# Performance work log

Hardware: AMD Instinct MI355X
Metric: run time of the kernel (lower is better)

Reference implementation:

```python
import jax, jax.numpy as jnp
import numpy as np

B, C, L = 64, 50, 128      # tactic states, context entries per state, AST tokens per entry
V, S = 100008, 128          # vocab (sum of id tables), state/embed dim
OUT = 3


def _gru(h, x, w_ih, w_hh, b_ih, b_hh):
    # torch.nn.GRUCell math
    gi = x @ w_ih.T + b_ih            # [N, 3S]
    gh = h @ w_hh.T + b_hh
    i_r, i_z, i_n = jnp.split(gi, 3, axis=-1)
    h_r, h_z, h_n = jnp.split(gh, 3, axis=-1)
    r = jax.nn.sigmoid(i_r + h_r)
    z = jax.nn.sigmoid(i_z + h_z)
    n = jnp.tanh(i_n + r * h_n)
    return (1.0 - z) * n + z * h


def setup_inputs() -> dict:
    key = jax.random.key(0)
    ks = jax.random.split(key, 16)
    def nrm(k, shape, scale=0.05):
        return jax.random.normal(k, shape, dtype=jnp.float32) * scale
    return {
        "token_ids": jax.random.randint(ks[0], (B, C, L), 0, V),
        "embed_table": nrm(ks[1], (V, S)),
        "ast_w_ih": nrm(ks[2], (3 * S, S)),
        "ast_w_hh": nrm(ks[3], (3 * S, S)),
        "ast_b_ih": nrm(ks[4], (3 * S,)),
        "ast_b_hh": nrm(ks[5], (3 * S,)),
        "ast_init": nrm(ks[6], (1, S)),
        "ctx_w_ih": nrm(ks[7], (3 * S, S)),
        "ctx_w_hh": nrm(ks[8], (3 * S, S)),
        "ctx_b_ih": nrm(ks[9], (3 * S,)),
        "ctx_b_hh": nrm(ks[10], (3 * S,)),
        "ctx_init": nrm(ks[11], (1, S)),
        "proj_w": nrm(ks[12], (S, S + 1)),
        "proj_b": nrm(ks[13], (S,)),
        "final_w": nrm(ks[14], (OUT, S)),
        "final_b": nrm(ks[15], (OUT,)),
    }


def reference(token_ids, embed_table, ast_w_ih, ast_w_hh, ast_b_ih, ast_b_hh,
              ast_init, ctx_w_ih, ctx_w_hh, ctx_b_ih, ctx_b_hh, ctx_init,
              proj_w, proj_b, final_w, final_b):
    Bv, Cv, Lv = token_ids.shape
    Sv = embed_table.shape[-1]
    # --- ast_embed: gather token embeddings, GRU over L steps, batched over B*C ---
    emb = embed_table[token_ids]                                  # [B,C,L,S]
    xs = emb.reshape(Bv * Cv, Lv, Sv).transpose(1, 0, 2)          # [L, B*C, S]
    h0 = jnp.broadcast_to(ast_init, (Bv * Cv, Sv))

    def ast_step(h, x):
        return _gru(h, x, ast_w_ih, ast_w_hh, ast_b_ih, ast_b_hh), None

    hT, _ = jax.lax.scan(ast_step, h0, xs)                        # [B*C, S]
    hT = hT.reshape(Bv, Cv, Sv)

    # --- mask: cat with conclusion indicator (1 for entry 0, else 0), then proj ---
    ind = (jnp.arange(Cv) == 0).astype(hT.dtype)[None, :, None]   # [1,C,1]
    ind = jnp.broadcast_to(ind, (Bv, Cv, 1))
    projs = jnp.concatenate([hT, ind], axis=-1) @ proj_w.T + proj_b  # [B,C,S]

    # --- ctx_embed: GRU over C context entries ---
    cxs = projs.transpose(1, 0, 2)                                # [C,B,S]
    c0 = jnp.broadcast_to(ctx_init, (Bv, Sv))

    def ctx_step(h, x):
        return _gru(h, x, ctx_w_ih, ctx_w_hh, ctx_b_ih, ctx_b_hh), None

    cT, _ = jax.lax.scan(ctx_step, c0, cxs)                       # [B,S]

    # --- final ---
    return cT @ final_w.T + final_b                               # [B,3]
```

## Files before the change

kernel.cpp:

```cpp
#include <hip/hip_runtime.h>


#define V_VOCAB 100008

typedef __attribute__((ext_vector_type(8))) short bf16x8;
typedef __attribute__((ext_vector_type(4))) float f32x4;

__device__ __forceinline__ unsigned pk_bf16(float lo, float hi){
  unsigned r;
  asm("v_cvt_pk_bf16_f32 %0, %1, %2" : "=v"(r) : "v"(lo), "v"(hi));
  return r;
}
__device__ __forceinline__ unsigned short bf1(float x){
  return (unsigned short)pk_bf16(x, x);
}
__device__ __forceinline__ bf16x8 pack8(f32x4 a, f32x4 b){
  union { unsigned u[4]; bf16x8 v; } x;
  x.u[0] = pk_bf16(a[0], a[1]);
  x.u[1] = pk_bf16(a[2], a[3]);
  x.u[2] = pk_bf16(b[0], b[1]);
  x.u[3] = pk_bf16(b[2], b[3]);
  return x.v;
}
__device__ __forceinline__ float bf2f(unsigned bits){
  union { unsigned u; float f; } x; x.u = bits << 16; return x.f;
}
__device__ __forceinline__ float fexp2(float x){ return __builtin_amdgcn_exp2f(x); }
__device__ __forceinline__ float frcp(float x){ return __builtin_amdgcn_rcpf(x); }
__device__ __forceinline__ float sigm(float x){ return frcp(1.f + fexp2(x * -1.44269504089f)); }
__device__ __forceinline__ float tanh_fast(float x){
  float t = fexp2(x * -2.88539008178f);
  return (1.f - t) * frcp(1.f + t);
}
__device__ __forceinline__ int hchunk(int row, int ch){
  return row*128 + ((ch ^ row ^ (row >> 2)) & 15)*8;
}

__global__ __launch_bounds__(256)
void m2_kernel(const float* __restrict__ wcih, const float* __restrict__ pw,
               const float* __restrict__ pb, const float* __restrict__ bcih,
               const float* __restrict__ bchh, float* __restrict__ M2,
               float* __restrict__ b2)
{
  int t = blockIdx.x*256 + threadIdx.x;
  if (t >= 384*130) return;
  int o = t / 130, kk = t % 130;
  const float* wr = wcih + o*128;
  if (kk < 129){
    float acc = 0.f;
    for (int m = 0; m < 128; ++m) acc += wr[m] * pw[m*129 + kk];
    M2[o*132 + kk] = acc;
  } else {
    float acc = bcih[o] + (o < 256 ? bchh[o] : 0.f);
    for (int m = 0; m < 128; ++m) acc += wr[m] * pb[m];
    b2[o] = acc;
  }
}

template<int STEPS, int DEPTH, bool EMB, bool FINAL>
__global__ __launch_bounds__(512, 1)
void gru_kernel(const int* __restrict__ tok_ids,
                const float* __restrict__ emb,
                const float* __restrict__ gi_f32,
                const float* __restrict__ whh,
                const float* __restrict__ wih,
                const float* __restrict__ bih,
                const float* __restrict__ bhh,
                const float* __restrict__ hinit,
                float* __restrict__ hout,
                const float* __restrict__ fw,
                const float* __restrict__ fb,
                float* __restrict__ outp)
{
  __shared__ unsigned short hbuf[2][2048];
  __shared__ int toks[EMB ? 2048 : 2];
  __shared__ unsigned short xbuf[EMB ? 4096 : 2];
  const int tid = threadIdx.x;
  const int w = tid >> 6, lane = tid & 63, c = lane & 15, q = lane >> 4;
  const int n0 = blockIdx.x * 16;
  const int w16c = w*16 + c;

  if constexpr (EMB){
    for (int i = tid; i < 2048; i += 512) toks[i] = tok_ids[n0*128 + i] << 9;
  }
  bf16x8 Bh[3][4], Bx[3][4];
#pragma unroll
  for (int g = 0; g < 3; ++g)
#pragma unroll
    for (int kt = 0; kt < 4; ++kt){
      int o = g*128 + w16c;
      const f32x4* ph = (const f32x4*)(whh + o*128 + kt*32 + q*8);
      Bh[g][kt] = pack8(ph[0], ph[1]);
      if constexpr (EMB){
        const f32x4* px = (const f32x4*)(wih + o*128 + kt*32 + q*8);
        Bx[g][kt] = pack8(px[0], px[1]);
      }
    }
  float cr, cz, cin;
  const float bn = bhh[256 + w16c];
  if constexpr (EMB){
    cr  = bih[w16c]       + bhh[w16c];
    cz  = bih[128 + w16c] + bhh[128 + w16c];
    cin = bih[256 + w16c];
  }
  float h_old[4];
  {
    float h0 = hinit[w16c];
#pragma unroll
    for (int r = 0; r < 4; ++r) h_old[r] = h0;
  }
  for (int i = tid; i < 2048; i += 512){
    int row = i >> 7, k = i & 127;
    hbuf[0][hchunk(row, k >> 3) + (k & 7)] = bf1(hinit[k]);
  }
  __syncthreads();

  if constexpr (EMB){
    const int srow = tid >> 5, spos = tid & 31;
    const int sdst = hchunk(srow, spos >> 1) + (spos & 1)*4;
    f32x4 E0, E1;
    auto load_x = [&](f32x4& E, int t){
      int tt = t < STEPS ? t : STEPS - 1;
      E = *(const f32x4*)((const char*)emb
            + (size_t)(unsigned)toks[srow*128 + tt] + spos*16);
    };
    auto write_x = [&](const f32x4& E, int b){
      unsigned long long v = ((unsigned long long)pk_bf16(E[2], E[3]) << 32)
                           | pk_bf16(E[0], E[1]);
      *(unsigned long long*)&xbuf[b*2048 + sdst] = v;
    };
    load_x(E0, 0);
    load_x(E1, 1);
    write_x(E0, 0);
    load_x(E0, 2);
    __syncthreads();

    auto body = [&](int s, f32x4& Ew){
      const int cur = s & 1, nxt = cur ^ 1;
      bf16x8 Ah[4], Ax[4];
#pragma unroll
      for (int kt = 0; kt < 4; ++kt){
        Ah[kt] = *(const bf16x8*)&hbuf[cur][hchunk(c, kt*4 + q)];
        Ax[kt] = *(const bf16x8*)&xbuf[cur*2048 + hchunk(c, kt*4 + q)];
      }
      f32x4 D0, D1, D2, D3;
#pragma unroll
      for (int r = 0; r < 4; ++r){ D0[r] = cr; D1[r] = cz; D2[r] = bn; D3[r] = cin; }
#pragma unroll
      for (int kt = 0; kt < 4; ++kt){
        D0 = __builtin_amdgcn_mfma_f32_16x16x32_bf16(Ax[kt], Bx[0][kt], D0, 0,0,0);
        D1 = __builtin_amdgcn_mfma_f32_16x16x32_bf16(Ax[kt], Bx[1][kt], D1, 0,0,0);
        D3 = __builtin_amdgcn_mfma_f32_16x16x32_bf16(Ax[kt], Bx[2][kt], D3, 0,0,0);
        D0 = __builtin_amdgcn_mfma_f32_16x16x32_bf16(Ah[kt], Bh[0][kt], D0, 0,0,0);
        D1 = __builtin_amdgcn_mfma_f32_16x16x32_bf16(Ah[kt], Bh[1][kt], D1, 0,0,0);
        D2 = __builtin_amdgcn_mfma_f32_16x16x32_bf16(Ah[kt], Bh[2][kt], D2, 0,0,0);
      }
      write_x(Ew, nxt);
      load_x(Ew, s + 3);
#pragma unroll
      for (int r = 0; r < 4; ++r){
        float rr = sigm(D0[r]);
        float z  = sigm(D1[r]);
        float nn = tanh_fast(D3[r] + rr * D2[r]);
        h_old[r] = nn + z*(h_old[r] - nn);
      }
#pragma unroll
      for (int r = 0; r < 4; ++r)
        hbuf[nxt][hchunk(q*4 + r, w*2 + (c >> 3)) + (c & 7)] = bf1(h_old[r]);
      asm volatile("s_waitcnt lgkmcnt(0)" ::: "memory");
      __builtin_amdgcn_s_barrier();
    };
#pragma unroll 1
    for (int s = 0; s < STEPS; s += 2){
      body(s,     E1);
      body(s + 1, E0);
    }
  } else {
    unsigned G[DEPTH][12];
    auto load_gi = [&](int d, int S){
#pragma unroll
      for (int r = 0; r < 4; ++r){
        const float* p = gi_f32 + (S*64 + n0 + q*4 + r)*384 + w16c;
        G[d][r]     = __float_as_uint(p[0]);
        G[d][4 + r] = __float_as_uint(p[128]);
        G[d][8 + r] = __float_as_uint(p[256]);
      }
    };
    auto body = [&](int S, int d){
      const int cur = S & 1, nxt = cur ^ 1;
      bf16x8 A[4];
#pragma unroll
      for (int kt = 0; kt < 4; ++kt)
        A[kt] = *(const bf16x8*)&hbuf[cur][hchunk(c, kt*4 + q)];
      f32x4 D[3];
#pragma unroll
      for (int r = 0; r < 4; ++r){
        D[0][r] = __uint_as_float(G[d][r]);
        D[1][r] = __uint_as_float(G[d][4 + r]);
        D[2][r] = bn;
      }
#pragma unroll
      for (int g = 0; g < 3; ++g)
#pragma unroll
        for (int kt = 0; kt < 4; ++kt)
          D[g] = __builtin_amdgcn_mfma_f32_16x16x32_bf16(A[kt], Bh[g][kt], D[g], 0,0,0);
#pragma unroll
      for (int r = 0; r < 4; ++r){
        float gn = __uint_as_float(G[d][8 + r]);
        float rr = sigm(D[0][r]);
        float z  = sigm(D[1][r]);
        float nn = tanh_fast(gn + rr * D[2][r]);
        h_old[r] = nn + z*(h_old[r] - nn);
      }
      if (S + DEPTH < STEPS) load_gi(d, S + DEPTH);
#pragma unroll
      for (int r = 0; r < 4; ++r)
        hbuf[nxt][hchunk(q*4 + r, w*2 + (c >> 3)) + (c & 7)] = bf1(h_old[r]);
      asm volatile("s_waitcnt lgkmcnt(0)" ::: "memory");
      __builtin_amdgcn_s_barrier();
    };
#pragma unroll
    for (int d = 0; d < DEPTH; ++d) load_gi(d, d);
#pragma unroll 1
    for (int s = 0; s < STEPS; s += DEPTH){
#pragma unroll
      for (int d = 0; d < DEPTH; ++d) body(s + d, d);
    }
  }

  if constexpr (FINAL){
    if (tid < 48){
      int row = tid / 3, j = tid % 3;
      float acc = fb[j];
      const int cur = STEPS & 1;
      for (int k = 0; k < 128; ++k)
        acc += bf2f(hbuf[cur][hchunk(row, k >> 3) + (k & 7)]) * fw[j*128 + k];
      outp[(n0 + row)*3 + j] = acc;
    }
  } else {
#pragma unroll
    for (int r = 0; r < 4; ++r)
      hout[(n0 + q*4 + r)*128 + w16c] = h_old[r];
  }
}

__global__ __launch_bounds__(256)
void cgi_kernel(const float* __restrict__ hT, const float* __restrict__ M2,
                const float* __restrict__ b2, float* __restrict__ cgi)
{
  const int tid = threadIdx.x;
  const int w = tid >> 6, lane = tid & 63, c = lane & 15, q = lane >> 4;
  const int n0 = (blockIdx.x*4 + w) * 16;
  bf16x8 A[4];
#pragma unroll
  for (int kt = 0; kt < 4; ++kt){
    const f32x4* p = (const f32x4*)(hT + (n0 + c)*128 + kt*32 + q*8);
    A[kt] = pack8(p[0], p[1]);
  }
#pragma unroll 1
  for (int ot = 0; ot < 24; ++ot){
    f32x4 D = {0.f,0.f,0.f,0.f};
#pragma unroll
    for (int kt = 0; kt < 4; ++kt){
      const f32x4* p = (const f32x4*)(M2 + (ot*16 + c)*132 + kt*32 + q*8);
      bf16x8 Bf = pack8(p[0], p[1]);
      D = __builtin_amdgcn_mfma_f32_16x16x32_bf16(A[kt], Bf, D, 0,0,0);
    }
    int o = ot*16 + c;
    float bias = b2[o];
    float indv = M2[o*132 + 128];
#pragma unroll
    for (int r = 0; r < 4; ++r){
      int n  = n0 + q*4 + r;
      int cc = n % 50, b = n / 50;
      float vv = D[r] + bias + (cc == 0 ? indv : 0.f);
      cgi[(cc*64 + b)*384 + o] = vv;
    }
  }
}

extern "C" void kernel_launch(void* const* d_in, const int* in_sizes, int n_in,
                              void* d_out, int out_size, void* d_ws, size_t ws_size,
                              hipStream_t stream)
{
  const int*   tok   = (const int*)  d_in[0];
  const float* emb   = (const float*)d_in[1];
  const float* awih  = (const float*)d_in[2];
  const float* awhh  = (const float*)d_in[3];
  const float* abih  = (const float*)d_in[4];
  const float* abhh  = (const float*)d_in[5];
  const float* ainit = (const float*)d_in[6];
  const float* cwih  = (const float*)d_in[7];
  const float* cwhh  = (const float*)d_in[8];
  const float* cbih  = (const float*)d_in[9];
  const float* cbhh  = (const float*)d_in[10];
  const float* cinit = (const float*)d_in[11];
  const float* pw    = (const float*)d_in[12];
  const float* pb    = (const float*)d_in[13];
  const float* fw    = (const float*)d_in[14];
  const float* fb    = (const float*)d_in[15];
  float* out = (float*)d_out;

  char* ws = (char*)d_ws;
  float* hT  = (float*)(ws + 0);
  float* cgi = (float*)(ws + 1638400);
  float* M2  = (float*)(ws + 6553600);
  float* b2  = (float*)(ws + 6756352);

  m2_kernel<<<195, 256, 0, stream>>>(cwih, pw, pb, cbih, cbhh, M2, b2);
  gru_kernel<128, 2, true,  false><<<200, 512, 0, stream>>>(
      tok, emb, nullptr, awhh, awih, abih, abhh, ainit, hT, nullptr, nullptr, nullptr);
  cgi_kernel<<<50, 256, 0, stream>>>(hT, M2, b2, cgi);
  gru_kernel<50,  2, false, true ><<<4,   512, 0, stream>>>(
      nullptr, nullptr, cgi, cwhh, nullptr, nullptr, cbhh, cinit, nullptr, fw, fb, out);
}
```

Baseline: 185.7 us.

## Halve GRU block to 4 waves, each computing two 16-column output tiles

The GRU kernels now run with 256 threads (4 waves) per block instead of 512, and each wave computes two 16-wide hidden-column tiles, so it holds twice as many weight fragments in registers. The embedding gather now loads 32 bytes per thread and packs 8 bf16 values per write. The aim is to cut per-step barrier cost across fewer waves and to reuse the A fragments over more MFMAs. In exchange each wave carries more register pressure and a longer serial MFMA chain per recurrent step, which may lengthen the critical path of the sequential recurrence.

Measured after the change: 214.4 us. +15.5%, slower.

```diff
diff --git a/kernel.cpp b/kernel.cpp
--- a/kernel.cpp
+++ b/kernel.cpp
@@ -58,7 +58,7 @@
 }
 
 template<int STEPS, int DEPTH, bool EMB, bool FINAL>
-__global__ __launch_bounds__(512, 1)
+__global__ __launch_bounds__(256, 1)
 void gru_kernel(const int* __restrict__ tok_ids,
                 const float* __restrict__ emb,
                 const float* __restrict__ gi_f32,
@@ -78,56 +78,58 @@
   const int tid = threadIdx.x;
   const int w = tid >> 6, lane = tid & 63, c = lane & 15, q = lane >> 4;
   const int n0 = blockIdx.x * 16;
-  const int w16c = w*16 + c;
 
   if constexpr (EMB){
-    for (int i = tid; i < 2048; i += 512) toks[i] = tok_ids[n0*128 + i] << 9;
-  }
-  bf16x8 Bh[3][4], Bx[3][4];
+    for (int i = tid; i < 2048; i += 256) toks[i] = tok_ids[n0*128 + i] << 9;
+  }
+  bf16x8 Bh[6][4], Bx[EMB ? 6 : 1][4];
 #pragma unroll
   for (int g = 0; g < 3; ++g)
 #pragma unroll
-    for (int kt = 0; kt < 4; ++kt){
-      int o = g*128 + w16c;
-      const f32x4* ph = (const f32x4*)(whh + o*128 + kt*32 + q*8);
-      Bh[g][kt] = pack8(ph[0], ph[1]);
-      if constexpr (EMB){
-        const f32x4* px = (const f32x4*)(wih + o*128 + kt*32 + q*8);
-        Bx[g][kt] = pack8(px[0], px[1]);
+    for (int jj = 0; jj < 2; ++jj)
+#pragma unroll
+      for (int kt = 0; kt < 4; ++kt){
+        int o = g*128 + w*32 + jj*16 + c;
+        const f32x4* ph = (const f32x4*)(whh + o*128 + kt*32 + q*8);
+        Bh[g*2+jj][kt] = pack8(ph[0], ph[1]);
+        if constexpr (EMB){
+          const f32x4* px = (const f32x4*)(wih + o*128 + kt*32 + q*8);
+          Bx[g*2+jj][kt] = pack8(px[0], px[1]);
+        }
       }
-    }
-  float cr, cz, cin;
-  const float bn = bhh[256 + w16c];
-  if constexpr (EMB){
-    cr  = bih[w16c]       + bhh[w16c];
-    cz  = bih[128 + w16c] + bhh[128 + w16c];
-    cin = bih[256 + w16c];
-  }
-  float h_old[4];
-  {
-    float h0 = hinit[w16c];
-#pragma unroll
-    for (int r = 0; r < 4; ++r) h_old[r] = h0;
-  }
-  for (int i = tid; i < 2048; i += 512){
+  float cr[2], cz[2], cin[2], bn[2];
+  float h_old[2][4];
+#pragma unroll
+  for (int jj = 0; jj < 2; ++jj){
+    int kc = w*32 + jj*16 + c;
+    bn[jj] = bhh[256 + kc];
+    if constexpr (EMB){
+      cr[jj]  = bih[kc]       + bhh[kc];
+      cz[jj]  = bih[128 + kc] + bhh[128 + kc];
+      cin[jj] = bih[256 + kc];
+    }
+    float h0 = hinit[kc];
+#pragma unroll
+    for (int r = 0; r < 4; ++r) h_old[jj][r] = h0;
+  }
+  for (int i = tid; i < 2048; i += 256){
     int row = i >> 7, k = i & 127;
     hbuf[0][hchunk(row, k >> 3) + (k & 7)] = bf1(hinit[k]);
   }
   __syncthreads();
 
   if constexpr (EMB){
-    const int srow = tid >> 5, spos = tid & 31;
-    const int sdst = hchunk(srow, spos >> 1) + (spos & 1)*4;
-    f32x4 E0, E1;
-    auto load_x = [&](f32x4& E, int t){
+    const int srow = tid >> 4, sch = tid & 15;
+    const int sdst = hchunk(srow, sch);
+    f32x4 E0[2], E1[2];
+    auto load_x = [&](f32x4 (&E)[2], int t){
       int tt = t < STEPS ? t : STEPS - 1;
-      E = *(const f32x4*)((const char*)emb
-            + (size_t)(unsigned)toks[srow*128 + tt] + spos*16);
-    };
-    auto write_x = [&](const f32x4& E, int b){
-      unsigned long long v = ((unsigned long long)pk_bf16(E[2], E[3]) << 32)
-                           | pk_bf16(E[0], E[1]);
-      *(unsigned long long*)&xbuf[b*2048 + sdst] = v;
+      const char* p = (const char*)emb + (size_t)(unsigned)toks[srow*128 + tt] + sch*32;
+      E[0] = *(const f32x4*)p;
+      E[1] = *(const f32x4*)(p + 16);
+    };
+    auto write_x = [&](const f32x4 (&E)[2], int b){
+      *(bf16x8*)&xbuf[b*2048 + sdst] = pack8(E[0], E[1]);
     };
     load_x(E0, 0);
     load_x(E1, 1);
@@ -135,7 +137,7 @@
     load_x(E0, 2);
     __syncthreads();
 
-    auto body = [&](int s, f32x4& Ew){
+    auto body = [&](int s, f32x4 (&Ew)[2]){
       const int cur = s & 1, nxt = cur ^ 1;
       bf16x8 Ah[4], Ax[4];
 #pragma unroll
@@ -143,30 +145,41 @@
         Ah[kt] = *(const bf16x8*)&hbuf[cur][hchunk(c, kt*4 + q)];
         Ax[kt] = *(const bf16x8*)&xbuf[cur*2048 + hchunk(c, kt*4 + q)];
       }
-      f32x4 D0, D1, D2, D3;
-#pragma unroll
-      for (int r = 0; r < 4; ++r){ D0[r] = cr; D1[r] = cz; D2[r] = bn; D3[r] = cin; }
-#pragma unroll
-      for (int kt = 0; kt < 4; ++kt){
-        D0 = __builtin_amdgcn_mfma_f32_16x16x32_bf16(Ax[kt], Bx[0][kt], D0, 0,0,0);
-        D1 = __builtin_amdgcn_mfma_f32_16x16x32_bf16(Ax[kt], Bx[1][kt], D1, 0,0,0);
-        D3 = __builtin_amdgcn_mfma_f32_16x16x32_bf16(Ax[kt], Bx[2][kt], D3, 0,0,0);
-        D0 = __builtin_amdgcn_mfma_f32_16x16x32_bf16(Ah[kt], Bh[0][kt], D0, 0,0,0);
-        D1 = __builtin_amdgcn_mfma_f32_16x16x32_bf16(Ah[kt], Bh[1][kt], D1, 0,0,0);
-        D2 = __builtin_amdgcn_mfma_f32_16x16x32_bf16(Ah[kt], Bh[2][kt], D2, 0,0,0);
-      }
+      f32x4 D0[2], D1[2], D2[2], D3[2];
+#pragma unroll
+      for (int jj = 0; jj < 2; ++jj)
+#pragma unroll
+        for (int r = 0; r < 4; ++r){
+          D0[jj][r] = cr[jj]; D1[jj][r] = cz[jj];
+          D2[jj][r] = bn[jj]; D3[jj][r] = cin[jj];
+        }
+#pragma unroll
+      for (int jj = 0; jj < 2; ++jj)
+#pragma unroll
+        for (int kt = 0; kt < 4; ++kt){
+          D0[jj] = __builtin_amdgcn_mfma_f32_16x16x32_bf16(Ax[kt], Bx[0+jj][kt], D0[jj], 0,0,0);
+          D1[jj] = __builtin_amdgcn_mfma_f32_16x16x32_bf16(Ax[kt], Bx[2+jj][kt], D1[jj], 0,0,0);
+          D3[jj] = __builtin_amdgcn_mfma_f32_16x16x32_bf16(Ax[kt], Bx[4+jj][kt], D3[jj], 0,0,0);
+          D0[jj] = __builtin_amdgcn_mfma_f32_16x16x32_bf16(Ah[kt], Bh[0+jj][kt], D0[jj], 0,0,0);
+          D1[jj] = __builtin_amdgcn_mfma_f32_16x16x32_bf16(Ah[kt], Bh[2+jj][kt], D1[jj], 0,0,0);
+          D2[jj] = __builtin_amdgcn_mfma_f32_16x16x32_bf16(Ah[kt], Bh[4+jj][kt], D2[jj], 0,0,0);
+        }
       write_x(Ew, nxt);
       load_x(Ew, s + 3);
 #pragma unroll
-      for (int r = 0; r < 4; ++r){
-        float rr = sigm(D0[r]);
-        float z  = sigm(D1[r]);
-        float nn = tanh_fast(D3[r] + rr * D2[r]);
-        h_old[r] = nn + z*(h_old[r] - nn);
-      }
-#pragma unroll
-      for (int r = 0; r < 4; ++r)
-        hbuf[nxt][hchunk(q*4 + r, w*2 + (c >> 3)) + (c & 7)] = bf1(h_old[r]);
+      for (int jj = 0; jj < 2; ++jj)
+#pragma unroll
+        for (int r = 0; r < 4; ++r){
+          float rr = sigm(D0[jj][r]);
+          float z  = sigm(D1[jj][r]);
+          float nn = tanh_fast(D3[jj][r] + rr * D2[jj][r]);
+          h_old[jj][r] = nn + z*(h_old[jj][r] - nn);
+        }
+#pragma unroll
+      for (int jj = 0; jj < 2; ++jj)
+#pragma unroll
+        for (int r = 0; r < 4; ++r)
+          hbuf[nxt][hchunk(q*4 + r, w*4 + jj*2 + (c >> 3)) + (c & 7)] = bf1(h_old[jj][r]);
       asm volatile("s_waitcnt lgkmcnt(0)" ::: "memory");
       __builtin_amdgcn_s_barrier();
     };
@@ -176,14 +189,16 @@
       body(s + 1, E0);
     }
   } else {
-    unsigned G[DEPTH][12];
+    unsigned G[DEPTH][24];
     auto load_gi = [&](int d, int S){
 #pragma unroll
       for (int r = 0; r < 4; ++r){
-        const float* p = gi_f32 + (S*64 + n0 + q*4 + r)*384 + w16c;
-        G[d][r]     = __float_as_uint(p[0]);
-        G[d][4 + r] = __float_as_uint(p[128]);
-        G[d][8 + r] = __float_as_uint(p[256]);
+        const float* p = gi_f32 + (S*64 + n0 + q*4 + r)*384 + w*32 + c;
+#pragma unroll
+        for (int g = 0; g < 3; ++g)
+#pragma unroll
+          for (int jj = 0; jj < 2; ++jj)
+            G[d][(g*2+jj)*4 + r] = __float_as_uint(p[g*128 + jj*16]);
       }
     };
     auto body = [&](int S, int d){
@@ -192,30 +207,39 @@
 #pragma unroll
       for (int kt = 0; kt < 4; ++kt)
         A[kt] = *(const bf16x8*)&hbuf[cur][hchunk(c, kt*4 + q)];
-      f32x4 D[3];
-#pragma unroll
-      for (int r = 0; r < 4; ++r){
-        D[0][r] = __uint_as_float(G[d][r]);
-        D[1][r] = __uint_as_float(G[d][4 + r]);
-        D[2][r] = bn;
-      }
-#pragma unroll
-      for (int g = 0; g < 3; ++g)
-#pragma unroll
-        for (int kt = 0; kt < 4; ++kt)
-          D[g] = __builtin_amdgcn_mfma_f32_16x16x32_bf16(A[kt], Bh[g][kt], D[g], 0,0,0);
-#pragma unroll
-      for (int r = 0; r < 4; ++r){
-        float gn = __uint_as_float(G[d][8 + r]);
-        float rr = sigm(D[0][r]);
-        float z  = sigm(D[1][r]);
-        float nn = tanh_fast(gn + rr * D[2][r]);
-        h_old[r] = nn + z*(h_old[r] - nn);
-      }
+      f32x4 D0[2], D1[2], D2[2];
+#pragma unroll
+      for (int jj = 0; jj < 2; ++jj)
+#pragma unroll
+        for (int r = 0; r < 4; ++r){
+          D0[jj][r] = __uint_as_float(G[d][(0+jj)*4 + r]);
+          D1[jj][r] = __uint_as_float(G[d][(2+jj)*4 + r]);
+          D2[jj][r] = bn[jj];
+        }
+#pragma unroll
+      for (int jj = 0; jj < 2; ++jj)
+#pragma unroll
+        for (int kt = 0; kt < 4; ++kt){
+          D0[jj] = __builtin_amdgcn_mfma_f32_16x16x32_bf16(A[kt], Bh[0+jj][kt], D0[jj], 0,0,0);
+          D1[jj] = __builtin_amdgcn_mfma_f32_16x16x32_bf16(A[kt], Bh[2+jj][kt], D1[jj], 0,0,0);
+          D2[jj] = __builtin_amdgcn_mfma_f32_16x16x32_bf16(A[kt], Bh[4+jj][kt], D2[jj], 0,0,0);
+        }
+#pragma unroll
+      for (int jj = 0; jj < 2; ++jj)
+#pragma unroll
+        for (int r = 0; r < 4; ++r){
+          float gn = __uint_as_float(G[d][(4+jj)*4 + r]);
+          float rr = sigm(D0[jj][r]);
+          float z  = sigm(D1[jj][r]);
+          float nn = tanh_fast(gn + rr * D2[jj][r]);
+          h_old[jj][r] = nn + z*(h_old[jj][r] - nn);
+        }
       if (S + DEPTH < STEPS) load_gi(d, S + DEPTH);
 #pragma unroll
-      for (int r = 0; r < 4; ++r)
-        hbuf[nxt][hchunk(q*4 + r, w*2 + (c >> 3)) + (c & 7)] = bf1(h_old[r]);
+      for (int jj = 0; jj < 2; ++jj)
+#pragma unroll
+        for (int r = 0; r < 4; ++r)
+          hbuf[nxt][hchunk(q*4 + r, w*4 + jj*2 + (c >> 3)) + (c & 7)] = bf1(h_old[jj][r]);
       asm volatile("s_waitcnt lgkmcnt(0)" ::: "memory");
       __builtin_amdgcn_s_barrier();
     };
@@ -239,8 +263,10 @@
     }
   } else {
 #pragma unroll
-    for (int r = 0; r < 4; ++r)
-      hout[(n0 + q*4 + r)*128 + w16c] = h_old[r];
+    for (int jj = 0; jj < 2; ++jj)
+#pragma unroll
+      for (int r = 0; r < 4; ++r)
+        hout[(n0 + q*4 + r)*128 + w*32 + jj*16 + c] = h_old[jj][r];
   }
 }
 
@@ -308,9 +334,9 @@
   float* b2  = (float*)(ws + 6756352);
 
   m2_kernel<<<195, 256, 0, stream>>>(cwih, pw, pb, cbih, cbhh, M2, b2);
-  gru_kernel<128, 2, true,  false><<<200, 512, 0, stream>>>(
+  gru_kernel<128, 2, true,  false><<<200, 256, 0, stream>>>(
       tok, emb, nullptr, awhh, awih, abih, abhh, ainit, hT, nullptr, nullptr, nullptr);
   cgi_kernel<<<50, 256, 0, stream>>>(hT, M2, b2, cgi);
-  gru_kernel<50,  2, false, true ><<<4,   512, 0, stream>>>(
+  gru_kernel<50,  2, false, true ><<<4,   256, 0, stream>>>(
       nullptr, nullptr, cgi, cwhh, nullptr, nullptr, cbhh, cinit, nullptr, fw, fb, out);
 }
```

## Prefetch next-step x operand into registers and issue input-gate MFMAs before h loads

Applied to the files above, without the earlier changes.

Restructures the AST GRU recurrence pipeline so that the x-side LDS fragment for step s+1 is read during step s and kept in registers. The input-gate MFMAs can then start right away at the beginning of each step, before the h-dependent LDS reads. The embedding prefetch is deepened to two steps ahead, with writes going into the current buffer. This is meant to take LDS latency off the serial critical path of each recurrence step. In exchange it costs extra VGPRs for the held fragments and a more intricate double-buffer ordering.

Result: faster. 181.5 us (-2.3%).

```diff
diff --git a/kernel.cpp b/kernel.cpp
--- a/kernel.cpp
+++ b/kernel.cpp
@@ -118,7 +118,7 @@
   if constexpr (EMB){
     const int srow = tid >> 5, spos = tid & 31;
     const int sdst = hchunk(srow, spos >> 1) + (spos & 1)*4;
-    f32x4 E0, E1;
+    f32x4 EA, EB, T0, T1;
     auto load_x = [&](f32x4& E, int t){
       int tt = t < STEPS ? t : STEPS - 1;
       E = *(const f32x4*)((const char*)emb
@@ -129,34 +129,45 @@
                            | pk_bf16(E[0], E[1]);
       *(unsigned long long*)&xbuf[b*2048 + sdst] = v;
     };
-    load_x(E0, 0);
-    load_x(E1, 1);
-    write_x(E0, 0);
-    load_x(E0, 2);
+    load_x(T0, 0);
+    load_x(T1, 1);
+    write_x(T0, 0);
+    write_x(T1, 1);
+    load_x(EA, 2);
+    load_x(EB, 3);
+    __syncthreads();
+    bf16x8 AxC[4], AxN[4];
+#pragma unroll
+    for (int kt = 0; kt < 4; ++kt)
+      AxC[kt] = *(const bf16x8*)&xbuf[hchunk(c, kt*4 + q)];
     __syncthreads();
 
     auto body = [&](int s, f32x4& Ew){
       const int cur = s & 1, nxt = cur ^ 1;
-      bf16x8 Ah[4], Ax[4];
+      f32x4 D0, D1, D2, D3;
+#pragma unroll
+      for (int r = 0; r < 4; ++r){ D0[r] = cr; D1[r] = cz; D2[r] = bn; D3[r] = cin; }
 #pragma unroll
       for (int kt = 0; kt < 4; ++kt){
+        D0 = __builtin_amdgcn_mfma_f32_16x16x32_bf16(AxC[kt], Bx[0][kt], D0, 0,0,0);
+        D1 = __builtin_amdgcn_mfma_f32_16x16x32_bf16(AxC[kt], Bx[1][kt], D1, 0,0,0);
+        D3 = __builtin_amdgcn_mfma_f32_16x16x32_bf16(AxC[kt], Bx[2][kt], D3, 0,0,0);
+      }
+      bf16x8 Ah[4];
+#pragma unroll
+      for (int kt = 0; kt < 4; ++kt)
         Ah[kt] = *(const bf16x8*)&hbuf[cur][hchunk(c, kt*4 + q)];
-        Ax[kt] = *(const bf16x8*)&xbuf[cur*2048 + hchunk(c, kt*4 + q)];
-      }
-      f32x4 D0, D1, D2, D3;
-#pragma unroll
-      for (int r = 0; r < 4; ++r){ D0[r] = cr; D1[r] = cz; D2[r] = bn; D3[r] = cin; }
 #pragma unroll
       for (int kt = 0; kt < 4; ++kt){
-        D0 = __builtin_amdgcn_mfma_f32_16x16x32_bf16(Ax[kt], Bx[0][kt], D0, 0,0,0);
-        D1 = __builtin_amdgcn_mfma_f32_16x16x32_bf16(Ax[kt], Bx[1][kt], D1, 0,0,0);
-        D3 = __builtin_amdgcn_mfma_f32_16x16x32_bf16(Ax[kt], Bx[2][kt], D3, 0,0,0);
         D0 = __builtin_amdgcn_mfma_f32_16x16x32_bf16(Ah[kt], Bh[0][kt], D0, 0,0,0);
         D1 = __builtin_amdgcn_mfma_f32_16x16x32_bf16(Ah[kt], Bh[1][kt], D1, 0,0,0);
         D2 = __builtin_amdgcn_mfma_f32_16x16x32_bf16(Ah[kt], Bh[2][kt], D2, 0,0,0);
       }
-      write_x(Ew, nxt);
-      load_x(Ew, s + 3);
+#pragma unroll
+      for (int kt = 0; kt < 4; ++kt)
+        AxN[kt] = *(const bf16x8*)&xbuf[nxt*2048 + hchunk(c, kt*4 + q)];
+      write_x(Ew, cur);
+      load_x(Ew, s + 4);
 #pragma unroll
       for (int r = 0; r < 4; ++r){
         float rr = sigm(D0[r]);
@@ -169,11 +180,13 @@
         hbuf[nxt][hchunk(q*4 + r, w*2 + (c >> 3)) + (c & 7)] = bf1(h_old[r]);
       asm volatile("s_waitcnt lgkmcnt(0)" ::: "memory");
       __builtin_amdgcn_s_barrier();
+#pragma unroll
+      for (int kt = 0; kt < 4; ++kt) AxC[kt] = AxN[kt];
     };
 #pragma unroll 1
     for (int s = 0; s < STEPS; s += 2){
-      body(s,     E1);
-      body(s + 1, E0);
+      body(s,     EA);
+      body(s + 1, EB);
     }
   } else {
     unsigned G[DEPTH][12];
```

## Load embeddings directly into MFMA fragments and precompute input gates a step ahead

Applied to the files above, without the earlier changes.

Removes the shared-memory staging buffer for token embeddings. Each lane now loads its own fp32 embedding slice straight into registers in the MFMA A-fragment layout and packs it to bf16. The input-side gate MFMAs (x·W_ih) for step s+1 run right after step s's nonlinearity, off the recurrent critical path, and their accumulators rotate between two register sets. This cuts LDS traffic and shortens the per-step dependency chain. In exchange, each lane issues more global loads (8 × 16B per step versus 1) and register pressure rises.

After: 316.0 us. 70.2% more time.

```diff
diff --git a/kernel.cpp b/kernel.cpp
--- a/kernel.cpp
+++ b/kernel.cpp
@@ -74,7 +74,6 @@
 {
   __shared__ unsigned short hbuf[2][2048];
   __shared__ int toks[EMB ? 2048 : 2];
-  __shared__ unsigned short xbuf[EMB ? 4096 : 2];
   const int tid = threadIdx.x;
   const int w = tid >> 6, lane = tid & 63, c = lane & 15, q = lane >> 4;
   const int n0 = blockIdx.x * 16;
@@ -116,54 +115,68 @@
   __syncthreads();
 
   if constexpr (EMB){
-    const int srow = tid >> 5, spos = tid & 31;
-    const int sdst = hchunk(srow, spos >> 1) + (spos & 1)*4;
-    f32x4 E0, E1;
-    auto load_x = [&](f32x4& E, int t){
+    f32x4 EF[8];
+    auto issue_x = [&](int t){
       int tt = t < STEPS ? t : STEPS - 1;
-      E = *(const f32x4*)((const char*)emb
-            + (size_t)(unsigned)toks[srow*128 + tt] + spos*16);
+      const char* pb = (const char*)emb + (size_t)(unsigned)toks[c*128 + tt] + q*32;
+#pragma unroll
+      for (int kt = 0; kt < 4; ++kt){
+        EF[2*kt]   = *(const f32x4*)(pb + kt*128);
+        EF[2*kt+1] = *(const f32x4*)(pb + kt*128 + 16);
+      }
     };
-    auto write_x = [&](const f32x4& E, int b){
-      unsigned long long v = ((unsigned long long)pk_bf16(E[2], E[3]) << 32)
-                           | pk_bf16(E[0], E[1]);
-      *(unsigned long long*)&xbuf[b*2048 + sdst] = v;
-    };
-    load_x(E0, 0);
-    load_x(E1, 1);
-    write_x(E0, 0);
-    load_x(E0, 2);
-    __syncthreads();
-
-    auto body = [&](int s, f32x4& Ew){
+    f32x4 P0, P1, P3, Q0, Q1, Q3;
+    issue_x(0);
+    {
+      bf16x8 AX[4];
+#pragma unroll
+      for (int kt = 0; kt < 4; ++kt) AX[kt] = pack8(EF[2*kt], EF[2*kt+1]);
+#pragma unroll
+      for (int r = 0; r < 4; ++r){ P0[r] = cr; P1[r] = cz; P3[r] = cin; }
+#pragma unroll
+      for (int kt = 0; kt < 4; ++kt){
+        P0 = __builtin_amdgcn_mfma_f32_16x16x32_bf16(AX[kt], Bx[0][kt], P0, 0,0,0);
+        P1 = __builtin_amdgcn_mfma_f32_16x16x32_bf16(AX[kt], Bx[1][kt], P1, 0,0,0);
+        P3 = __builtin_amdgcn_mfma_f32_16x16x32_bf16(AX[kt], Bx[2][kt], P3, 0,0,0);
+      }
+    }
+    issue_x(1);
+
+    auto body = [&](int s, f32x4& C0, f32x4& C1, f32x4& C3,
+                           f32x4& N0, f32x4& N1, f32x4& N3){
       const int cur = s & 1, nxt = cur ^ 1;
-      bf16x8 Ah[4], Ax[4];
+      bf16x8 Ah[4];
+#pragma unroll
+      for (int kt = 0; kt < 4; ++kt)
+        Ah[kt] = *(const bf16x8*)&hbuf[cur][hchunk(c, kt*4 + q)];
+      f32x4 D2;
+#pragma unroll
+      for (int r = 0; r < 4; ++r) D2[r] = bn;
 #pragma unroll
       for (int kt = 0; kt < 4; ++kt){
-        Ah[kt] = *(const bf16x8*)&hbuf[cur][hchunk(c, kt*4 + q)];
-        Ax[kt] = *(const bf16x8*)&xbuf[cur*2048 + hchunk(c, kt*4 + q)];
-      }
-      f32x4 D0, D1, D2, D3;
-#pragma unroll
-      for (int r = 0; r < 4; ++r){ D0[r] = cr; D1[r] = cz; D2[r] = bn; D3[r] = cin; }
+        C0 = __builtin_amdgcn_mfma_f32_16x16x32_bf16(Ah[kt], Bh[0][kt], C0, 0,0,0);
+        C1 = __builtin_amdgcn_mfma_f32_16x16x32_bf16(Ah[kt], Bh[1][kt], C1, 0,0,0);
+        D2 = __builtin_amdgcn_mfma_f32_16x16x32_bf16(Ah[kt], Bh[2][kt], D2, 0,0,0);
+      }
+#pragma unroll
+      for (int r = 0; r < 4; ++r){
+        float rr = sigm(C0[r]);
+        float z  = sigm(C1[r]);
+        float nn = tanh_fast(C3[r] + rr * D2[r]);
+        h_old[r] = nn + z*(h_old[r] - nn);
+      }
+      bf16x8 AX[4];
+#pragma unroll
+      for (int kt = 0; kt < 4; ++kt) AX[kt] = pack8(EF[2*kt], EF[2*kt+1]);
+#pragma unroll
+      for (int r = 0; r < 4; ++r){ N0[r] = cr; N1[r] = cz; N3[r] = cin; }
 #pragma unroll
       for (int kt = 0; kt < 4; ++kt){
-        D0 = __builtin_amdgcn_mfma_f32_16x16x32_bf16(Ax[kt], Bx[0][kt], D0, 0,0,0);
-        D1 = __builtin_amdgcn_mfma_f32_16x16x32_bf16(Ax[kt], Bx[1][kt], D1, 0,0,0);
-        D3 = __builtin_amdgcn_mfma_f32_16x16x32_bf16(Ax[kt], Bx[2][kt], D3, 0,0,0);
-        D0 = __builtin_amdgcn_mfma_f32_16x16x32_bf16(Ah[kt], Bh[0][kt], D0, 0,0,0);
-        D1 = __builtin_amdgcn_mfma_f32_16x16x32_bf16(Ah[kt], Bh[1][kt], D1, 0,0,0);
-        D2 = __builtin_amdgcn_mfma_f32_16x16x32_bf16(Ah[kt], Bh[2][kt], D2, 0,0,0);
-      }
-      write_x(Ew, nxt);
-      load_x(Ew, s + 3);
-#pragma unroll
-      for (int r = 0; r < 4; ++r){
-        float rr = sigm(D0[r]);
-        float z  = sigm(D1[r]);
-        float nn = tanh_fast(D3[r] + rr * D2[r]);
-        h_old[r] = nn + z*(h_old[r] - nn);
-      }
+        N0 = __builtin_amdgcn_mfma_f32_16x16x32_bf16(AX[kt], Bx[0][kt], N0, 0,0,0);
+        N1 = __builtin_amdgcn_mfma_f32_16x16x32_bf16(AX[kt], Bx[1][kt], N1, 0,0,0);
+        N3 = __builtin_amdgcn_mfma_f32_16x16x32_bf16(AX[kt], Bx[2][kt], N3, 0,0,0);
+      }
+      issue_x(s + 2);
 #pragma unroll
       for (int r = 0; r < 4; ++r)
         hbuf[nxt][hchunk(q*4 + r, w*2 + (c >> 3)) + (c & 7)] = bf1(h_old[r]);
@@ -172,8 +185,8 @@
     };
 #pragma unroll 1
     for (int s = 0; s < STEPS; s += 2){
-      body(s,     E1);
-      body(s + 1, E0);
+      body(s,     P0, P1, P3, Q0, Q1, Q3);
+      body(s + 1, Q0, Q1, Q3, P0, P1, P3);
     }
   } else {
     unsigned G[DEPTH][12];
```
